# Kernel tuning notes

Measured on AMD Instinct MI355X. Metric: run time of the kernel, lower is better.

## Reference

```python
import jax, jax.numpy as jnp
import numpy as np

N_NODES = 4096
HIDDEN = 64
N_REL = 8
N_LAYERS = 2


def setup_inputs() -> dict:
    key = jax.random.key(0)
    k0, k1, k2, k3, k4 = jax.random.split(key, 5)
    node_embed = jax.random.normal(k0, (N_NODES + 1, HIDDEN), dtype=jnp.float32)
    w_self = jax.random.normal(k1, (N_LAYERS, HIDDEN, HIDDEN), dtype=jnp.float32) * 0.02
    w_rel = jax.random.normal(k2, (N_LAYERS, N_REL, HIDDEN, HIDDEN), dtype=jnp.float32) * 0.02
    # dense per-relation adjacency buffer [R, N, N]
    rel_adj = jax.random.uniform(k3, (N_REL, N_NODES, N_NODES), dtype=jnp.float32)
    keyword_ids = jax.random.randint(k4, (64, 32), 0, N_NODES + 1)  # pad id == N_NODES
    return {"node_embed": node_embed, "w_self": w_self, "w_rel": w_rel,
            "rel_adj": rel_adj, "keyword_ids": keyword_ids}


def reference(node_embed, w_self, w_rel, rel_adj, keyword_ids):
    num_nodes = rel_adj.shape[1]
    h = node_embed[:num_nodes]  # [N, D]
    for l in range(w_self.shape[0]):
        out = h @ w_self[l]                                   # self loop [N, D]
        msg = jnp.einsum('rnm,md->rnd', rel_adj, h)           # per-relation aggregation
        out = out + jnp.einsum('rnd,rde->ne', msg, w_rel[l])  # per-relation projection, summed over r
        h = jax.nn.relu(out)
    pad = jnp.zeros((1, h.shape[1]), dtype=h.dtype)
    full_plus_pad = jnp.concatenate([h, pad], axis=0)  # [N+1, D]
    return full_plus_pad[keyword_ids]                  # [B, K, D]
```

## Files before the change

### kernel.cpp

```cpp
#include <hip/hip_runtime.h>

#define N_NODES 4096
#define HID 64
#define NH (N_NODES * HID)

typedef float f32x4 __attribute__((ext_vector_type(4)));
typedef short s16x8 __attribute__((ext_vector_type(8)));

__device__ __forceinline__ short f2bf(float f) {
    union { float f; unsigned u; } v; v.f = f;
    unsigned r = v.u + 0x7fffu + ((v.u >> 16) & 1u);
    return (short)(r >> 16);
}

__global__ __launch_bounds__(256) void proj_kernel(
    const float* __restrict__ h, const float* __restrict__ w_self_l,
    const float* __restrict__ w_rel_l, float* __restrict__ S,
    short* __restrict__ BT)
{
    __shared__ float hs[64][65];
    __shared__ float wt[64][64];
    const int tid = threadIdx.x;
    const int mb = blockIdx.x;
    const int p = blockIdx.y;
    const float* w = (p < 8) ? (w_rel_l + p * 64 * 64) : w_self_l;

    #pragma unroll
    for (int i = 0; i < 4; ++i) {
        int idx4 = tid + 256 * i;
        int row = idx4 >> 4, c = idx4 & 15;
        float4 v = *((const float4*)(h + (size_t)(mb * 64 + row) * HID) + c);
        hs[row][c * 4 + 0] = v.x; hs[row][c * 4 + 1] = v.y;
        hs[row][c * 4 + 2] = v.z; hs[row][c * 4 + 3] = v.w;
    }
    #pragma unroll
    for (int i = 0; i < 4; ++i) {
        int idx4 = tid + 256 * i;
        ((float4*)wt)[idx4] = ((const float4*)w)[idx4];
    }
    __syncthreads();

    const int m = tid & 63;
    const int eb = (tid >> 6) * 16;
    float acc[16];
    #pragma unroll
    for (int j = 0; j < 16; ++j) acc[j] = 0.f;

    #pragma unroll 4
    for (int d = 0; d < 64; ++d) {
        float hv = hs[m][d];
        const float4* wr = (const float4*)&wt[d][eb];
        float4 w0 = wr[0], w1 = wr[1], w2 = wr[2], w3 = wr[3];
        acc[0]  += hv * w0.x; acc[1]  += hv * w0.y; acc[2]  += hv * w0.z; acc[3]  += hv * w0.w;
        acc[4]  += hv * w1.x; acc[5]  += hv * w1.y; acc[6]  += hv * w1.z; acc[7]  += hv * w1.w;
        acc[8]  += hv * w2.x; acc[9]  += hv * w2.y; acc[10] += hv * w2.z; acc[11] += hv * w2.w;
        acc[12] += hv * w3.x; acc[13] += hv * w3.y; acc[14] += hv * w3.z; acc[15] += hv * w3.w;
    }

    if (p < 8) {
        #pragma unroll
        for (int j = 0; j < 16; ++j)
            BT[(size_t)(p * 64 + eb + j) * N_NODES + mb * 64 + m] = f2bf(acc[j]);
    } else {
        #pragma unroll
        for (int j = 0; j < 16; ++j)
            S[(size_t)(mb * 64 + m) * HID + eb + j] = acc[j];
    }
}

__global__ __launch_bounds__(256) void gemm_kernel(
    const float* __restrict__ A, const short* __restrict__ BT,
    float* __restrict__ msg)
{
    const int tid = threadIdx.x;
    const int gid = blockIdx.x;
    const int r  = gid & 7;
    const int rb = (gid >> 3) & 63;
    const int ks = gid >> 9;
    const int wave = tid >> 6, lane = tid & 63;
    const int quad = lane >> 4, l16 = lane & 15;

    const int row = rb * 64 + wave * 16 + l16;
    const float* arow = A + ((size_t)r * N_NODES + row) * N_NODES + ks * 2048 + quad * 8;
    const short* bbase = BT + ((size_t)r * 64 + l16) * N_NODES + ks * 2048 + quad * 8;

    f32x4 acc[4];
    #pragma unroll
    for (int nb = 0; nb < 4; ++nb) acc[nb] = (f32x4){0.f, 0.f, 0.f, 0.f};

    #pragma unroll 2
    for (int k = 0; k < 2048; k += 32) {
        f32x4 a0 = __builtin_nontemporal_load((const f32x4*)(arow + k));
        f32x4 a1 = __builtin_nontemporal_load((const f32x4*)(arow + k + 4));
        s16x8 af;
        af[0] = f2bf(a0[0]); af[1] = f2bf(a0[1]); af[2] = f2bf(a0[2]); af[3] = f2bf(a0[3]);
        af[4] = f2bf(a1[0]); af[5] = f2bf(a1[1]); af[6] = f2bf(a1[2]); af[7] = f2bf(a1[3]);
        #pragma unroll
        for (int nb = 0; nb < 4; ++nb) {
            s16x8 bfr = *(const s16x8*)(bbase + (size_t)nb * 16 * N_NODES + k);
            acc[nb] = __builtin_amdgcn_mfma_f32_16x16x32_bf16(af, bfr, acc[nb], 0, 0, 0);
        }
    }

    float* mo = msg + ((size_t)(r * 2 + ks)) * NH;
    #pragma unroll
    for (int nb = 0; nb < 4; ++nb) {
        #pragma unroll
        for (int i = 0; i < 4; ++i) {
            int orow = rb * 64 + wave * 16 + quad * 4 + i;
            mo[(size_t)orow * HID + nb * 16 + l16] = acc[nb][i];
        }
    }
}

__global__ __launch_bounds__(256) void relu_kernel(
    const float* __restrict__ S, const float* __restrict__ msg, float* __restrict__ hout)
{
    int i = blockIdx.x * 256 + threadIdx.x;
    float4 s = ((const float4*)S)[i];
    #pragma unroll
    for (int p = 0; p < 16; ++p) {
        float4 m = ((const float4*)(msg + (size_t)p * NH))[i];
        s.x += m.x; s.y += m.y; s.z += m.z; s.w += m.w;
    }
    float4 o;
    o.x = fmaxf(s.x, 0.f); o.y = fmaxf(s.y, 0.f);
    o.z = fmaxf(s.z, 0.f); o.w = fmaxf(s.w, 0.f);
    ((float4*)hout)[i] = o;
}

__global__ __launch_bounds__(256) void gather_kernel(
    const float* __restrict__ h2, const int* __restrict__ kw, float* __restrict__ out)
{
    int e = blockIdx.x * 256 + threadIdx.x;
    int ki = e >> 6, d = e & 63;
    int id = kw[ki];
    out[e] = ((unsigned)id < (unsigned)N_NODES) ? h2[(size_t)id * HID + d] : 0.f;
}

extern "C" void kernel_launch(void* const* d_in, const int* in_sizes, int n_in,
                              void* d_out, int out_size, void* d_ws, size_t ws_size,
                              hipStream_t stream) {
    const float* node_embed = (const float*)d_in[0];
    const float* w_self     = (const float*)d_in[1];
    const float* w_rel      = (const float*)d_in[2];
    const float* rel_adj    = (const float*)d_in[3];
    const int*   kw         = (const int*)d_in[4];
    float* out = (float*)d_out;

    float* msg = (float*)d_ws;
    float* S   = msg + 16 * NH;
    float* h1  = S + NH;
    float* h2  = h1 + NH;
    short* BT  = (short*)(h2 + NH);

    const float* hin = node_embed;
    float* houts[2] = {h1, h2};
    for (int l = 0; l < 2; ++l) {
        proj_kernel<<<dim3(64, 9), 256, 0, stream>>>(
            hin, w_self + (size_t)l * 64 * 64, w_rel + (size_t)l * 8 * 64 * 64, S, BT);
        gemm_kernel<<<1024, 256, 0, stream>>>(rel_adj, BT, msg);
        relu_kernel<<<256, 256, 0, stream>>>(S, msg, houts[l]);
        hin = houts[l];
    }
    gather_kernel<<<512, 256, 0, stream>>>(h2, kw, out);
}
```

Baseline: 976.2 us.

## Stage adjacency and projected tiles through LDS with register prefetch in gemm

The gemm kernel now loads 64x64 tiles of the fp32 adjacency and the bf16 projected features cooperatively into shared memory, using row-contiguous 16-byte loads. The next tile is prefetched into registers while the current one is consumed by MFMAs. The old per-lane strided global reads are replaced by coalesced row loads, aimed at better DRAM efficiency on this bandwidth-bound stream of 512MB of adjacency per layer. The cost is two barriers per k-step plus LDS traffic, and a launch-bounds occupancy hint is added.

```diff
diff --git a/kernel.cpp b/kernel.cpp
--- a/kernel.cpp
+++ b/kernel.cpp
@@ -68,10 +68,13 @@
     }
 }
 
-__global__ __launch_bounds__(256) void gemm_kernel(
+__global__ __launch_bounds__(256, 4) void gemm_kernel(
     const float* __restrict__ A, const short* __restrict__ BT,
     float* __restrict__ msg)
 {
+    __shared__ float As[64][68];
+    __shared__ short Bs[64][72];
+
     const int tid = threadIdx.x;
     const int gid = blockIdx.x;
     const int r  = gid & 7;
@@ -80,25 +83,58 @@
     const int wave = tid >> 6, lane = tid & 63;
     const int quad = lane >> 4, l16 = lane & 15;
 
-    const int row = rb * 64 + wave * 16 + l16;
-    const float* arow = A + ((size_t)r * N_NODES + row) * N_NODES + ks * 2048 + quad * 8;
-    const short* bbase = BT + ((size_t)r * 64 + l16) * N_NODES + ks * 2048 + quad * 8;
+    const int rA = tid >> 4, cA = tid & 15;
+    const int rB = tid >> 3, cB = tid & 7;
+    const float* Ag = A  + ((size_t)r * N_NODES + rb * 64) * N_NODES + ks * 2048;
+    const short* Bg = BT + ((size_t)r * 64) * N_NODES + ks * 2048;
 
     f32x4 acc[4];
     #pragma unroll
     for (int nb = 0; nb < 4; ++nb) acc[nb] = (f32x4){0.f, 0.f, 0.f, 0.f};
 
-    #pragma unroll 2
-    for (int k = 0; k < 2048; k += 32) {
-        f32x4 a0 = __builtin_nontemporal_load((const f32x4*)(arow + k));
-        f32x4 a1 = __builtin_nontemporal_load((const f32x4*)(arow + k + 4));
-        s16x8 af;
-        af[0] = f2bf(a0[0]); af[1] = f2bf(a0[1]); af[2] = f2bf(a0[2]); af[3] = f2bf(a0[3]);
-        af[4] = f2bf(a1[0]); af[5] = f2bf(a1[1]); af[6] = f2bf(a1[2]); af[7] = f2bf(a1[3]);
-        #pragma unroll
-        for (int nb = 0; nb < 4; ++nb) {
-            s16x8 bfr = *(const s16x8*)(bbase + (size_t)nb * 16 * N_NODES + k);
-            acc[nb] = __builtin_amdgcn_mfma_f32_16x16x32_bf16(af, bfr, acc[nb], 0, 0, 0);
+    f32x4 a_reg[4];
+    s16x8 b_reg[2];
+    #pragma unroll
+    for (int j = 0; j < 4; ++j)
+        a_reg[j] = __builtin_nontemporal_load(
+            (const f32x4*)(Ag + (size_t)(rA + 16 * j) * N_NODES + cA * 4));
+    #pragma unroll
+    for (int j = 0; j < 2; ++j)
+        b_reg[j] = *(const s16x8*)(Bg + (size_t)(rB + 32 * j) * N_NODES + cB * 8);
+
+    for (int kk = 0; kk < 32; ++kk) {
+        __syncthreads();
+        #pragma unroll
+        for (int j = 0; j < 4; ++j)
+            *(f32x4*)&As[rA + 16 * j][cA * 4] = a_reg[j];
+        #pragma unroll
+        for (int j = 0; j < 2; ++j)
+            *(s16x8*)&Bs[rB + 32 * j][cB * 8] = b_reg[j];
+
+        if (kk < 31) {
+            const int k0 = (kk + 1) * 64;
+            #pragma unroll
+            for (int j = 0; j < 4; ++j)
+                a_reg[j] = __builtin_nontemporal_load(
+                    (const f32x4*)(Ag + (size_t)(rA + 16 * j) * N_NODES + k0 + cA * 4));
+            #pragma unroll
+            for (int j = 0; j < 2; ++j)
+                b_reg[j] = *(const s16x8*)(Bg + (size_t)(rB + 32 * j) * N_NODES + k0 + cB * 8);
+        }
+        __syncthreads();
+
+        #pragma unroll
+        for (int s = 0; s < 2; ++s) {
+            f32x4 af0 = *(const f32x4*)&As[wave * 16 + l16][s * 32 + quad * 8];
+            f32x4 af1 = *(const f32x4*)&As[wave * 16 + l16][s * 32 + quad * 8 + 4];
+            s16x8 af;
+            af[0] = f2bf(af0[0]); af[1] = f2bf(af0[1]); af[2] = f2bf(af0[2]); af[3] = f2bf(af0[3]);
+            af[4] = f2bf(af1[0]); af[5] = f2bf(af1[1]); af[6] = f2bf(af1[2]); af[7] = f2bf(af1[3]);
+            #pragma unroll
+            for (int nb = 0; nb < 4; ++nb) {
+                s16x8 bfr = *(const s16x8*)&Bs[l16 + nb * 16][s * 32 + quad * 8];
+                acc[nb] = __builtin_amdgcn_mfma_f32_16x16x32_bf16(af, bfr, acc[nb], 0, 0, 0);
+            }
         }
     }
 
```

New measurement: 825.5 us. 1.18x faster.

## Stage GEMM tiles through double-buffered LDS via direct global-to-LDS loads

Applied to the files above, without the earlier changes.

The adjacency GEMM now copies A (fp32) and B (bf16) tiles straight into LDS with the global_load_lds builtin. It uses two buffers, so loading the next 64-wide k-slice overlaps the MFMA work on the current one. An XOR swizzle on the chunk index avoids LDS bank conflicts, and the launch bounds now ask for 3 blocks per SM. The kernel is bandwidth-bound on streaming the 512MB fp32 adjacency. The change aims for better latency hiding and coalesced fetches, at the cost of LDS use, per-step barriers, and the loss of nontemporal load hints.

```diff
diff --git a/kernel.cpp b/kernel.cpp
--- a/kernel.cpp
+++ b/kernel.cpp
@@ -12,6 +12,10 @@
     unsigned r = v.u + 0x7fffu + ((v.u >> 16) & 1u);
     return (short)(r >> 16);
 }
+
+#define GLOAD_LDS16(g, l) __builtin_amdgcn_global_load_lds( \
+    (const __attribute__((address_space(1))) unsigned int*)(g), \
+    (__attribute__((address_space(3))) unsigned int*)(l), 16, 0, 0)
 
 __global__ __launch_bounds__(256) void proj_kernel(
     const float* __restrict__ h, const float* __restrict__ w_self_l,
@@ -68,10 +72,13 @@
     }
 }
 
-__global__ __launch_bounds__(256) void gemm_kernel(
+__global__ __launch_bounds__(256, 3) void gemm_kernel(
     const float* __restrict__ A, const short* __restrict__ BT,
     float* __restrict__ msg)
 {
+    __shared__ __attribute__((aligned(16))) float As[2][4096];
+    __shared__ __attribute__((aligned(16))) short Bs[2][4096];
+
     const int tid = threadIdx.x;
     const int gid = blockIdx.x;
     const int r  = gid & 7;
@@ -80,26 +87,57 @@
     const int wave = tid >> 6, lane = tid & 63;
     const int quad = lane >> 4, l16 = lane & 15;
 
-    const int row = rb * 64 + wave * 16 + l16;
-    const float* arow = A + ((size_t)r * N_NODES + row) * N_NODES + ks * 2048 + quad * 8;
-    const short* bbase = BT + ((size_t)r * 64 + l16) * N_NODES + ks * 2048 + quad * 8;
+    const float* Ag = A  + ((size_t)r * N_NODES + rb * 64) * N_NODES + ks * 2048;
+    const short* Bg = BT + ((size_t)r * 64) * N_NODES + ks * 2048;
 
     f32x4 acc[4];
     #pragma unroll
     for (int nb = 0; nb < 4; ++nb) acc[nb] = (f32x4){0.f, 0.f, 0.f, 0.f};
 
-    #pragma unroll 2
-    for (int k = 0; k < 2048; k += 32) {
-        f32x4 a0 = __builtin_nontemporal_load((const f32x4*)(arow + k));
-        f32x4 a1 = __builtin_nontemporal_load((const f32x4*)(arow + k + 4));
-        s16x8 af;
-        af[0] = f2bf(a0[0]); af[1] = f2bf(a0[1]); af[2] = f2bf(a0[2]); af[3] = f2bf(a0[3]);
-        af[4] = f2bf(a1[0]); af[5] = f2bf(a1[1]); af[6] = f2bf(a1[2]); af[7] = f2bf(a1[3]);
-        #pragma unroll
-        for (int nb = 0; nb < 4; ++nb) {
-            s16x8 bfr = *(const s16x8*)(bbase + (size_t)nb * 16 * N_NODES + k);
-            acc[nb] = __builtin_amdgcn_mfma_f32_16x16x32_bf16(af, bfr, acc[nb], 0, 0, 0);
-        }
+    auto stage = [&](int b, int t) {
+        const int k0 = t * 64;
+        #pragma unroll
+        for (int j = 0; j < 4; ++j) {
+            int region = wave + j * 4;
+            int row = region * 4 + (lane >> 4);
+            int sc  = lane & 15;
+            int gch = ((((sc >> 1) ^ (row & 7)) << 1) | (sc & 1));
+            GLOAD_LDS16(Ag + (size_t)row * N_NODES + k0 + gch * 4,
+                        &As[b][region * 256]);
+        }
+        #pragma unroll
+        for (int j = 0; j < 2; ++j) {
+            int region = wave + j * 4;
+            int e  = region * 8 + (lane >> 3);
+            int sc = lane & 7;
+            int gch = sc ^ (e & 7);
+            GLOAD_LDS16(Bg + (size_t)e * N_NODES + k0 + gch * 8,
+                        &Bs[b][region * 512]);
+        }
+    };
+
+    stage(0, 0);
+    __syncthreads();
+
+    for (int t = 0; t < 32; ++t) {
+        const int b = t & 1;
+        if (t < 31) stage(b ^ 1, t + 1);
+
+        #pragma unroll
+        for (int s = 0; s < 2; ++s) {
+            int sp = (s * 4 + quad) ^ (l16 & 7);
+            const f32x4* ap = (const f32x4*)&As[b][(wave * 16 + l16) * 64 + sp * 8];
+            f32x4 af0 = ap[0], af1 = ap[1];
+            s16x8 af;
+            af[0] = f2bf(af0[0]); af[1] = f2bf(af0[1]); af[2] = f2bf(af0[2]); af[3] = f2bf(af0[3]);
+            af[4] = f2bf(af1[0]); af[5] = f2bf(af1[1]); af[6] = f2bf(af1[2]); af[7] = f2bf(af1[3]);
+            #pragma unroll
+            for (int nb = 0; nb < 4; ++nb) {
+                s16x8 bfr = *(const s16x8*)&Bs[b][(nb * 16 + l16) * 64 + sp * 8];
+                acc[nb] = __builtin_amdgcn_mfma_f32_16x16x32_bf16(af, bfr, acc[nb], 0, 0, 0);
+            }
+        }
+        __syncthreads();
     }
 
     float* mo = msg + ((size_t)(r * 2 + ks)) * NH;
```

Result: faster. 875.8 us (-10.3%).

## Restructure adjacency GEMM into single-wave blocks with coalesced LDS-staged A loads

Applied to the files above, without the earlier changes.

The adjacency GEMM now runs one 64-lane wave per block, and each block covers 16 rows over the full K range instead of splitting K in two. A tiles are read as coalesced row chunks, converted to bf16 and staged through double-buffered LDS, with register prefetch two steps ahead and sched_barriers to order the loads, LDS writes and MFMAs. Dropping the K split halves the partial message buffers and the relu reduction work. The trade-off is more blocks with less parallelism per block, and B fragments are reloaded from global memory by every block.

```diff
diff --git a/kernel.cpp b/kernel.cpp
--- a/kernel.cpp
+++ b/kernel.cpp
@@ -3,8 +3,10 @@
 #define N_NODES 4096
 #define HID 64
 #define NH (N_NODES * HID)
+#define NPART 8
 
 typedef float f32x4 __attribute__((ext_vector_type(4)));
+typedef short s16x4 __attribute__((ext_vector_type(4)));
 typedef short s16x8 __attribute__((ext_vector_type(8)));
 
 __device__ __forceinline__ short f2bf(float f) {
@@ -68,49 +70,102 @@
     }
 }
 
-__global__ __launch_bounds__(256) void gemm_kernel(
+__global__ __launch_bounds__(64, 2) void gemm_kernel(
     const float* __restrict__ A, const short* __restrict__ BT,
     float* __restrict__ msg)
 {
-    const int tid = threadIdx.x;
+    __shared__ __attribute__((aligned(16))) short As[2][16 * 72];
+
     const int gid = blockIdx.x;
     const int r  = gid & 7;
-    const int rb = (gid >> 3) & 63;
-    const int ks = gid >> 9;
-    const int wave = tid >> 6, lane = tid & 63;
+    const int mg = gid >> 3;
+    const int lane = threadIdx.x;
     const int quad = lane >> 4, l16 = lane & 15;
-
-    const int row = rb * 64 + wave * 16 + l16;
-    const float* arow = A + ((size_t)r * N_NODES + row) * N_NODES + ks * 2048 + quad * 8;
-    const short* bbase = BT + ((size_t)r * 64 + l16) * N_NODES + ks * 2048 + quad * 8;
+    const int rowL = lane >> 2, ch = lane & 3;
+
+    const float* Ag = A + ((size_t)r * N_NODES + mg * 16 + rowL) * (size_t)N_NODES
+                        + ch * 4;
+    const short* Bg = BT + ((size_t)r * 64 + l16) * (size_t)N_NODES + quad * 8;
 
     f32x4 acc[4];
     #pragma unroll
     for (int nb = 0; nb < 4; ++nb) acc[nb] = (f32x4){0.f, 0.f, 0.f, 0.f};
 
-    #pragma unroll 2
-    for (int k = 0; k < 2048; k += 32) {
-        f32x4 a0 = __builtin_nontemporal_load((const f32x4*)(arow + k));
-        f32x4 a1 = __builtin_nontemporal_load((const f32x4*)(arow + k + 4));
-        s16x8 af;
-        af[0] = f2bf(a0[0]); af[1] = f2bf(a0[1]); af[2] = f2bf(a0[2]); af[3] = f2bf(a0[3]);
-        af[4] = f2bf(a1[0]); af[5] = f2bf(a1[1]); af[6] = f2bf(a1[2]); af[7] = f2bf(a1[3]);
-        #pragma unroll
-        for (int nb = 0; nb < 4; ++nb) {
-            s16x8 bfr = *(const s16x8*)(bbase + (size_t)nb * 16 * N_NODES + k);
-            acc[nb] = __builtin_amdgcn_mfma_f32_16x16x32_bf16(af, bfr, acc[nb], 0, 0, 0);
-        }
-    }
-
-    float* mo = msg + ((size_t)(r * 2 + ks)) * NH;
+    f32x4 Ra[4], Rb[4];
+
+#define ALOAD(RS, T) do {                                                     \
+    const float* _ap = Ag + (T) * 64;                                         \
+    RS[0] = __builtin_nontemporal_load((const f32x4*)(_ap));                  \
+    RS[1] = __builtin_nontemporal_load((const f32x4*)(_ap + 16));             \
+    RS[2] = __builtin_nontemporal_load((const f32x4*)(_ap + 32));             \
+    RS[3] = __builtin_nontemporal_load((const f32x4*)(_ap + 48));             \
+} while (0)
+
+#define AWRITE(RS, BUF) do {                                                  \
+    short* _ab = &As[BUF][rowL * 72 + ch * 4];                                \
+    s16x4 _v;                                                                 \
+    _v[0]=f2bf(RS[0][0]); _v[1]=f2bf(RS[0][1]); _v[2]=f2bf(RS[0][2]); _v[3]=f2bf(RS[0][3]); \
+    *(s16x4*)(_ab +  0) = _v;                                                 \
+    _v[0]=f2bf(RS[1][0]); _v[1]=f2bf(RS[1][1]); _v[2]=f2bf(RS[1][2]); _v[3]=f2bf(RS[1][3]); \
+    *(s16x4*)(_ab + 16) = _v;                                                 \
+    _v[0]=f2bf(RS[2][0]); _v[1]=f2bf(RS[2][1]); _v[2]=f2bf(RS[2][2]); _v[3]=f2bf(RS[2][3]); \
+    *(s16x4*)(_ab + 32) = _v;                                                 \
+    _v[0]=f2bf(RS[3][0]); _v[1]=f2bf(RS[3][1]); _v[2]=f2bf(RS[3][2]); _v[3]=f2bf(RS[3][3]); \
+    *(s16x4*)(_ab + 48) = _v;                                                 \
+} while (0)
+
+#define ITER(U, CUR, NXT, BC, BW) do {                                        \
+             \
+    const short* _bp = Bg + (U) * 64;                                         \
+    s16x8 b00 = *(const s16x8*)(_bp);                                         \
+    s16x8 b01 = *(const s16x8*)(_bp + 32);                                    \
+    s16x8 b10 = *(const s16x8*)(_bp + 16 * N_NODES);                          \
+    s16x8 b11 = *(const s16x8*)(_bp + 16 * N_NODES + 32);                     \
+    s16x8 b20 = *(const s16x8*)(_bp + 32 * N_NODES);                          \
+    s16x8 b21 = *(const s16x8*)(_bp + 32 * N_NODES + 32);                     \
+    s16x8 b30 = *(const s16x8*)(_bp + 48 * N_NODES);                          \
+    s16x8 b31 = *(const s16x8*)(_bp + 48 * N_NODES + 32);                     \
+    __builtin_amdgcn_sched_barrier(0);                                        \
+              \
+    if ((U) + 2 < 64) ALOAD(NXT, (U) + 2);                                    \
+    __builtin_amdgcn_sched_barrier(0);                                        \
+          \
+    if ((U) + 1 < 64) AWRITE(CUR, BW);                                        \
+    __builtin_amdgcn_sched_barrier(0);                                        \
+                                           \
+    {                                                                         \
+        s16x8 af0 = *(const s16x8*)&As[BC][l16 * 72 +      quad * 8];         \
+        s16x8 af1 = *(const s16x8*)&As[BC][l16 * 72 + 32 + quad * 8];         \
+        acc[0] = __builtin_amdgcn_mfma_f32_16x16x32_bf16(af0, b00, acc[0], 0, 0, 0); \
+        acc[0] = __builtin_amdgcn_mfma_f32_16x16x32_bf16(af1, b01, acc[0], 0, 0, 0); \
+        acc[1] = __builtin_amdgcn_mfma_f32_16x16x32_bf16(af0, b10, acc[1], 0, 0, 0); \
+        acc[1] = __builtin_amdgcn_mfma_f32_16x16x32_bf16(af1, b11, acc[1], 0, 0, 0); \
+        acc[2] = __builtin_amdgcn_mfma_f32_16x16x32_bf16(af0, b20, acc[2], 0, 0, 0); \
+        acc[2] = __builtin_amdgcn_mfma_f32_16x16x32_bf16(af1, b21, acc[2], 0, 0, 0); \
+        acc[3] = __builtin_amdgcn_mfma_f32_16x16x32_bf16(af0, b30, acc[3], 0, 0, 0); \
+        acc[3] = __builtin_amdgcn_mfma_f32_16x16x32_bf16(af1, b31, acc[3], 0, 0, 0); \
+    }                                                                         \
+} while (0)
+
+    ALOAD(Ra, 0);
+    AWRITE(Ra, 0);
+    ALOAD(Rb, 1);
+
+    for (int uu = 0; uu < 64; uu += 2) {
+        ITER(uu,     Rb, Ra, 0, 1);
+        ITER(uu + 1, Ra, Rb, 1, 0);
+    }
+
+    float* mo = msg + (size_t)r * NH + ((size_t)mg * 16) * HID;
     #pragma unroll
     for (int nb = 0; nb < 4; ++nb) {
         #pragma unroll
-        for (int i = 0; i < 4; ++i) {
-            int orow = rb * 64 + wave * 16 + quad * 4 + i;
-            mo[(size_t)orow * HID + nb * 16 + l16] = acc[nb][i];
-        }
-    }
+        for (int i = 0; i < 4; ++i)
+            mo[(size_t)(quad * 4 + i) * HID + nb * 16 + l16] = acc[nb][i];
+    }
+#undef ITER
+#undef AWRITE
+#undef ALOAD
 }
 
 __global__ __launch_bounds__(256) void relu_kernel(
@@ -119,7 +174,7 @@
     int i = blockIdx.x * 256 + threadIdx.x;
     float4 s = ((const float4*)S)[i];
     #pragma unroll
-    for (int p = 0; p < 16; ++p) {
+    for (int p = 0; p < NPART; ++p) {
         float4 m = ((const float4*)(msg + (size_t)p * NH))[i];
         s.x += m.x; s.y += m.y; s.z += m.z; s.w += m.w;
     }
@@ -149,7 +204,7 @@
     float* out = (float*)d_out;
 
     float* msg = (float*)d_ws;
-    float* S   = msg + 16 * NH;
+    float* S   = msg + NPART * NH;
     float* h1  = S + NH;
     float* h2  = h1 + NH;
     short* BT  = (short*)(h2 + NH);
@@ -159,7 +214,7 @@
     for (int l = 0; l < 2; ++l) {
         proj_kernel<<<dim3(64, 9), 256, 0, stream>>>(
             hin, w_self + (size_t)l * 64 * 64, w_rel + (size_t)l * 8 * 64 * 64, S, BT);
-        gemm_kernel<<<1024, 256, 0, stream>>>(rel_adj, BT, msg);
+        gemm_kernel<<<2048, 64, 0, stream>>>(rel_adj, BT, msg);
         relu_kernel<<<256, 256, 0, stream>>>(S, msg, houts[l]);
         hin = houts[l];
     }
```

Measured after the change: 928.1 us. 1.05x faster.
